# Performance work log

Hardware: AMD Instinct MI355X
Metric: run time of the kernel (lower is better)

The kernel has to match this reference:

```python
import jax, jax.numpy as jnp
import numpy as np

N_LAYER = 2
DEPTH = 2
D_IN = 64
H1 = 64
N = 8192  # sequence length; H2 == N is required by F * chord_mask


def make_chord(n):
    # eye(n) plus, for k in {0,1}, mask[i, (i + 2^k - 1) % n] = 1
    # k=0 re-sets the diagonal; k=1 sets the (wrapped) superdiagonal.
    eye = jnp.eye(n, dtype=jnp.float32)
    superdiag = jnp.roll(eye, 1, axis=1)  # [i, (i+1)%n] = 1
    return jnp.minimum(eye + superdiag, 1.0)


def setup_inputs() -> dict:
    key = jax.random.key(0)
    ks = jax.random.split(key, 8)
    s_in = 1.0 / np.sqrt(D_IN)
    X = jax.random.normal(ks[0], (N, D_IN), dtype=jnp.float32)
    # g stack: DEPTH x Linear(D_IN -> H1) (requires H1 == D_IN to stack)
    g_w = jax.random.uniform(ks[1], (DEPTH, H1, D_IN), jnp.float32, -s_in, s_in)
    g_b = jax.random.uniform(ks[2], (DEPTH, H1), jnp.float32, -s_in, s_in)
    # f stacks, one per layer m: (DEPTH-1) x Linear(D_IN->D_IN), then Linear(D_IN->H2=N)
    f0_w = jax.random.uniform(ks[3], (N_LAYER, D_IN, D_IN), jnp.float32, -s_in, s_in)
    f0_b = jax.random.uniform(ks[4], (N_LAYER, D_IN), jnp.float32, -s_in, s_in)
    fL_w = jax.random.uniform(ks[5], (N_LAYER, N, D_IN), jnp.float32, -s_in, s_in)
    fL_b = jax.random.uniform(ks[6], (N_LAYER, N), jnp.float32, -s_in, s_in)
    return {"X": X, "g_w": g_w, "g_b": g_b, "f0_w": f0_w, "f0_b": f0_b,
            "fL_w": fL_w, "fL_b": fL_b}


def reference(X, g_w, g_b, f0_w, f0_b, fL_w, fL_b):
    chord_mask = make_chord(N)  # [N, N], ~2 nonzeros per row
    # V0 = g stack applied to X
    V = X
    for d in range(DEPTH):
        V = jax.nn.relu(V @ g_w[d].T + g_b[d])  # [N, H1]
    # chained masked-score matmuls
    for m in range(N_LAYER):
        F = jax.nn.relu(X @ f0_w[m].T + f0_b[m])   # [N, D_IN]
        F = jax.nn.relu(F @ fL_w[m].T + fL_b[m])   # [N, N] dense score
        W = F * chord_mask                          # chord-sparse
        V = W @ V                                   # [N, H1]
    return V
```

## Files before the change

kernel.cpp:

```cpp
#include <hip/hip_runtime.h>


#define NROWS 8192
#define BROWS 16
#define RPW 5

__device__ __forceinline__ float rl(float v, int lane) {
  return __int_as_float(__builtin_amdgcn_readlane(__float_as_int(v), lane));
}

__device__ __forceinline__ float wave_sum(float x) {
  x += __int_as_float(__builtin_amdgcn_update_dpp(0, __float_as_int(x), 0x121, 0xF, 0xF, false));
  x += __int_as_float(__builtin_amdgcn_update_dpp(0, __float_as_int(x), 0x122, 0xF, 0xF, false));
  x += __int_as_float(__builtin_amdgcn_update_dpp(0, __float_as_int(x), 0x124, 0xF, 0xF, false));
  x += __int_as_float(__builtin_amdgcn_update_dpp(0, __float_as_int(x), 0x128, 0xF, 0xF, false));
  float a0 = rl(x, 0), a1 = rl(x, 16), a2 = rl(x, 32), a3 = rl(x, 48);
  return (a0 + a1) + (a2 + a3);
}

__device__ __forceinline__ void stageW2(float4 (*Wq)[16][65],
                                        const float* __restrict__ W, int tid) {
  const float4* ws = (const float4*)W;
#pragma unroll
  for (int p = 0; p < 8; ++p) {
    int idx = p * 256 + tid;
    int rem = idx & 1023;
    Wq[idx >> 10][rem & 15][rem >> 4] = ws[idx];
  }
}

template <int R>
__device__ __forceinline__ void mm64_s(const float4 (*Wq)[65], int lane,
                                       const float* __restrict__ X,
                                       const int* growu, float bias, float* acc) {
#pragma unroll
  for (int r = 0; r < R; ++r) acc[r] = bias;
#pragma unroll 4
  for (int kb = 0; kb < 16; ++kb) {
    float4 w4 = Wq[kb][lane];
#pragma unroll
    for (int r = 0; r < R; ++r) {
      float4 xq = *(const float4*)(X + (growu[r] << 6) + (kb << 2));
      acc[r] = fmaf(xq.x, w4.x, acc[r]);
      acc[r] = fmaf(xq.y, w4.y, acc[r]);
      acc[r] = fmaf(xq.z, w4.z, acc[r]);
      acc[r] = fmaf(xq.w, w4.w, acc[r]);
    }
  }
#pragma unroll
  for (int r = 0; r < R; ++r) acc[r] = fmaxf(acc[r], 0.0f);
}

template <int R>
__device__ __forceinline__ void mm64_rl(const float4 (*Wq)[65], int lane,
                                        const float* src, float bias, float* acc) {
#pragma unroll
  for (int r = 0; r < R; ++r) acc[r] = bias;
#pragma unroll 4
  for (int kb = 0; kb < 16; ++kb) {
    float4 w4 = Wq[kb][lane];
#pragma unroll
    for (int r = 0; r < R; ++r) {
      acc[r] = fmaf(rl(src[r], 4 * kb + 0), w4.x, acc[r]);
      acc[r] = fmaf(rl(src[r], 4 * kb + 1), w4.y, acc[r]);
      acc[r] = fmaf(rl(src[r], 4 * kb + 2), w4.z, acc[r]);
      acc[r] = fmaf(rl(src[r], 4 * kb + 3), w4.w, acc[r]);
    }
  }
#pragma unroll
  for (int r = 0; r < R; ++r) acc[r] = fmaxf(acc[r], 0.0f);
}

__global__ __launch_bounds__(256, 2) void fused_smfnet(
    const float* __restrict__ X, const float* __restrict__ g_w,
    const float* __restrict__ g_b, const float* __restrict__ f0_w,
    const float* __restrict__ f0_b, const float* __restrict__ fL_w,
    const float* __restrict__ fL_b, float* __restrict__ out)
{
  __shared__ float4 Wq[2][16][65];
  __shared__ float V0s[20][65];
  __shared__ float V1s[17][65];

  const int tid  = threadIdx.x;
  const int lane = tid & 63;
  const int wv   = tid >> 6;
  const int r0   = blockIdx.x * BROWS;

  stageW2(Wq, g_w, tid);
  float hb  = g_b[lane];
  float vb  = g_b[64 + lane];

  int growu[RPW];
#pragma unroll
  for (int r = 0; r < RPW; ++r) {
    int L = wv * RPW + r;
    growu[r] = __builtin_amdgcn_readfirstlane((r0 + L) & (NROWS - 1));
  }
  __syncthreads();

  float h[RPW];
  mm64_s<RPW>(Wq[0], lane, X, growu, hb, h);

  float v0[RPW];
  mm64_rl<RPW>(Wq[1], lane, h, vb, v0);
#pragma unroll
  for (int r = 0; r < RPW; ++r) V0s[wv * RPW + r][lane] = v0[r];

  __syncthreads();
  stageW2(Wq, f0_w, tid);
  __syncthreads();

  float tb0 = f0_b[lane];
  float t[RPW];
  mm64_s<RPW>(Wq[0], lane, X, growu, tb0, t);

  float v1[RPW];
#pragma unroll
  for (int r = 0; r < RPW; ++r) {
    int L = wv * RPW + r;
    if (L <= 16) {
      int g   = growu[r];
      int gp1 = (g + 1) & (NROWS - 1);
      float pa = wave_sum(t[r] * fL_w[g * 64 + lane]);
      float pb = wave_sum(t[r] * fL_w[gp1 * 64 + lane]);
      float a  = fmaxf(pa + fL_b[g], 0.0f);
      float b  = fmaxf(pb + fL_b[gp1], 0.0f);
      v1[r] = a * v0[r] + b * V0s[L + 1][lane];
      V1s[L][lane] = v1[r];
    }
  }

  __syncthreads();
  float tb1 = f0_b[64 + lane];
  mm64_s<RPW>(Wq[1], lane, X, growu, tb1, t);

  const float* fw1 = fL_w + NROWS * 64;
  const float* fb1 = fL_b + NROWS;
#pragma unroll
  for (int r = 0; r < RPW; ++r) {
    int L = wv * RPW + r;
    if (L <= 15) {
      int g   = growu[r];
      int gp1 = (g + 1) & (NROWS - 1);
      float pa = wave_sum(t[r] * fw1[g * 64 + lane]);
      float pb = wave_sum(t[r] * fw1[gp1 * 64 + lane]);
      float a  = fmaxf(pa + fb1[g], 0.0f);
      float b  = fmaxf(pb + fb1[gp1], 0.0f);
      out[g * 64 + lane] = a * v1[r] + b * V1s[L + 1][lane];
    }
  }
}

extern "C" void kernel_launch(void* const* d_in, const int* in_sizes, int n_in,
                              void* d_out, int out_size, void* d_ws, size_t ws_size,
                              hipStream_t stream) {
  const float* X    = (const float*)d_in[0];
  const float* g_w  = (const float*)d_in[1];
  const float* g_b  = (const float*)d_in[2];
  const float* f0_w = (const float*)d_in[3];
  const float* f0_b = (const float*)d_in[4];
  const float* fL_w = (const float*)d_in[5];
  const float* fL_b = (const float*)d_in[6];
  float* out = (float*)d_out;

  fused_smfnet<<<dim3(NROWS / BROWS), dim3(256), 0, stream>>>(
      X, g_w, g_b, f0_w, f0_b, fL_w, fL_b, out);
}
```

Measured before the change: 85.11 us.

## Prefetch weights into registers, fuse f0 matmuls, and stage h through LDS

Global loads for g_w, f0_w and the fL_w rows each thread needs are issued up front into registers, so their latency overlaps the first matmuls instead of sitting between barriers. The two f0 layer matmuls are fused into one pass that shares the X loads. The second g layer now reads h from shared memory instead of using a readlane per element. The wave reduction uses row_bcast DPP steps rather than four readlanes. Holding the prefetched values in registers raises register pressure under launch_bounds(256,2) and may cause spills.

```diff
diff --git a/kernel.cpp b/kernel.cpp
--- a/kernel.cpp
+++ b/kernel.cpp
@@ -9,24 +9,20 @@
   return __int_as_float(__builtin_amdgcn_readlane(__float_as_int(v), lane));
 }
 
+template <int CTRL, int ROWMASK>
+__device__ __forceinline__ float dppadd(float x) {
+  return __int_as_float(__builtin_amdgcn_update_dpp(
+      0, __float_as_int(x), CTRL, ROWMASK, 0xF, false));
+}
+
 __device__ __forceinline__ float wave_sum(float x) {
-  x += __int_as_float(__builtin_amdgcn_update_dpp(0, __float_as_int(x), 0x121, 0xF, 0xF, false));
-  x += __int_as_float(__builtin_amdgcn_update_dpp(0, __float_as_int(x), 0x122, 0xF, 0xF, false));
-  x += __int_as_float(__builtin_amdgcn_update_dpp(0, __float_as_int(x), 0x124, 0xF, 0xF, false));
-  x += __int_as_float(__builtin_amdgcn_update_dpp(0, __float_as_int(x), 0x128, 0xF, 0xF, false));
-  float a0 = rl(x, 0), a1 = rl(x, 16), a2 = rl(x, 32), a3 = rl(x, 48);
-  return (a0 + a1) + (a2 + a3);
-}
-
-__device__ __forceinline__ void stageW2(float4 (*Wq)[16][65],
-                                        const float* __restrict__ W, int tid) {
-  const float4* ws = (const float4*)W;
-#pragma unroll
-  for (int p = 0; p < 8; ++p) {
-    int idx = p * 256 + tid;
-    int rem = idx & 1023;
-    Wq[idx >> 10][rem & 15][rem >> 4] = ws[idx];
-  }
+  x += dppadd<0x121, 0xF>(x);
+  x += dppadd<0x122, 0xF>(x);
+  x += dppadd<0x124, 0xF>(x);
+  x += dppadd<0x128, 0xF>(x);
+  x += dppadd<0x142, 0xA>(x);
+  x += dppadd<0x143, 0xC>(x);
+  return rl(x, 63);
 }
 
 template <int R>
@@ -52,8 +48,39 @@
 }
 
 template <int R>
-__device__ __forceinline__ void mm64_rl(const float4 (*Wq)[65], int lane,
-                                        const float* src, float bias, float* acc) {
+__device__ __forceinline__ void mm64_x2(const float4 (*W0)[65], const float4 (*W1)[65],
+                                        int lane, const float* __restrict__ X,
+                                        const int* growu, float b0, float b1,
+                                        float* a0, float* a1) {
+#pragma unroll
+  for (int r = 0; r < R; ++r) { a0[r] = b0; a1[r] = b1; }
+#pragma unroll 4
+  for (int kb = 0; kb < 16; ++kb) {
+    float4 w0 = W0[kb][lane];
+    float4 w1 = W1[kb][lane];
+#pragma unroll
+    for (int r = 0; r < R; ++r) {
+      float4 xq = *(const float4*)(X + (growu[r] << 6) + (kb << 2));
+      a0[r] = fmaf(xq.x, w0.x, a0[r]);
+      a0[r] = fmaf(xq.y, w0.y, a0[r]);
+      a0[r] = fmaf(xq.z, w0.z, a0[r]);
+      a0[r] = fmaf(xq.w, w0.w, a0[r]);
+      a1[r] = fmaf(xq.x, w1.x, a1[r]);
+      a1[r] = fmaf(xq.y, w1.y, a1[r]);
+      a1[r] = fmaf(xq.z, w1.z, a1[r]);
+      a1[r] = fmaf(xq.w, w1.w, a1[r]);
+    }
+  }
+#pragma unroll
+  for (int r = 0; r < R; ++r) {
+    a0[r] = fmaxf(a0[r], 0.0f);
+    a1[r] = fmaxf(a1[r], 0.0f);
+  }
+}
+
+template <int R>
+__device__ __forceinline__ void mm64_h(const float4 (*Wq)[65], int lane,
+                                       const float (*Hrow)[64], float bias, float* acc) {
 #pragma unroll
   for (int r = 0; r < R; ++r) acc[r] = bias;
 #pragma unroll 4
@@ -61,10 +88,11 @@
     float4 w4 = Wq[kb][lane];
 #pragma unroll
     for (int r = 0; r < R; ++r) {
-      acc[r] = fmaf(rl(src[r], 4 * kb + 0), w4.x, acc[r]);
-      acc[r] = fmaf(rl(src[r], 4 * kb + 1), w4.y, acc[r]);
-      acc[r] = fmaf(rl(src[r], 4 * kb + 2), w4.z, acc[r]);
-      acc[r] = fmaf(rl(src[r], 4 * kb + 3), w4.w, acc[r]);
+      float4 hq = *(const float4*)(&Hrow[r][kb << 2]);
+      acc[r] = fmaf(hq.x, w4.x, acc[r]);
+      acc[r] = fmaf(hq.y, w4.y, acc[r]);
+      acc[r] = fmaf(hq.z, w4.z, acc[r]);
+      acc[r] = fmaf(hq.w, w4.w, acc[r]);
     }
   }
 #pragma unroll
@@ -80,70 +108,93 @@
   __shared__ float4 Wq[2][16][65];
   __shared__ float V0s[20][65];
   __shared__ float V1s[17][65];
+  __shared__ __align__(16) float Hs[4][RPW][64];
 
   const int tid  = threadIdx.x;
   const int lane = tid & 63;
   const int wv   = tid >> 6;
   const int r0   = blockIdx.x * BROWS;
 
-  stageW2(Wq, g_w, tid);
-  float hb  = g_b[lane];
-  float vb  = g_b[64 + lane];
+  const float4* gq = (const float4*)g_w;
+  float4 gw[8];
+#pragma unroll
+  for (int p = 0; p < 8; ++p) gw[p] = gq[p * 256 + tid];
 
   int growu[RPW];
 #pragma unroll
+  for (int r = 0; r < RPW; ++r)
+    growu[r] = __builtin_amdgcn_readfirstlane((r0 + wv * RPW + r) & (NROWS - 1));
+
+  const float* fw1 = fL_w + NROWS * 64;
+  float fa0[RPW], fb0[RPW], fa1[RPW], fb1v[RPW];
+#pragma unroll
   for (int r = 0; r < RPW; ++r) {
-    int L = wv * RPW + r;
-    growu[r] = __builtin_amdgcn_readfirstlane((r0 + L) & (NROWS - 1));
-  }
+    int g = growu[r], gp1 = (g + 1) & (NROWS - 1);
+    fa0[r]  = fL_w[g * 64 + lane];
+    fb0[r]  = fL_w[gp1 * 64 + lane];
+    fa1[r]  = fw1[g * 64 + lane];
+    fb1v[r] = fw1[gp1 * 64 + lane];
+  }
+
+  const float4* fq = (const float4*)f0_w;
+  float4 fw[8];
+#pragma unroll
+  for (int p = 0; p < 8; ++p) fw[p] = fq[p * 256 + tid];
+
+#pragma unroll
+  for (int p = 0; p < 8; ++p) {
+    int idx = p * 256 + tid, rem = idx & 1023;
+    Wq[idx >> 10][rem & 15][rem >> 4] = gw[p];
+  }
+  float hb = g_b[lane], vb = g_b[64 + lane];
   __syncthreads();
 
   float h[RPW];
   mm64_s<RPW>(Wq[0], lane, X, growu, hb, h);
+#pragma unroll
+  for (int r = 0; r < RPW; ++r) Hs[wv][r][lane] = h[r];
 
   float v0[RPW];
-  mm64_rl<RPW>(Wq[1], lane, h, vb, v0);
+  mm64_h<RPW>(Wq[1], lane, Hs[wv], vb, v0);
 #pragma unroll
   for (int r = 0; r < RPW; ++r) V0s[wv * RPW + r][lane] = v0[r];
-
-  __syncthreads();
-  stageW2(Wq, f0_w, tid);
-  __syncthreads();
-
-  float tb0 = f0_b[lane];
-  float t[RPW];
-  mm64_s<RPW>(Wq[0], lane, X, growu, tb0, t);
+  __syncthreads();
+
+#pragma unroll
+  for (int p = 0; p < 8; ++p) {
+    int idx = p * 256 + tid, rem = idx & 1023;
+    Wq[idx >> 10][rem & 15][rem >> 4] = fw[p];
+  }
+  __syncthreads();
+
+  float t0[RPW], t1[RPW];
+  mm64_x2<RPW>(Wq[0], Wq[1], lane, X, growu,
+               f0_b[lane], f0_b[64 + lane], t0, t1);
 
   float v1[RPW];
 #pragma unroll
   for (int r = 0; r < RPW; ++r) {
     int L = wv * RPW + r;
     if (L <= 16) {
-      int g   = growu[r];
-      int gp1 = (g + 1) & (NROWS - 1);
-      float pa = wave_sum(t[r] * fL_w[g * 64 + lane]);
-      float pb = wave_sum(t[r] * fL_w[gp1 * 64 + lane]);
+      int g = growu[r], gp1 = (g + 1) & (NROWS - 1);
+      float pa = wave_sum(t0[r] * fa0[r]);
+      float pb = wave_sum(t0[r] * fb0[r]);
       float a  = fmaxf(pa + fL_b[g], 0.0f);
       float b  = fmaxf(pb + fL_b[gp1], 0.0f);
       v1[r] = a * v0[r] + b * V0s[L + 1][lane];
       V1s[L][lane] = v1[r];
     }
   }
-
-  __syncthreads();
-  float tb1 = f0_b[64 + lane];
-  mm64_s<RPW>(Wq[1], lane, X, growu, tb1, t);
-
-  const float* fw1 = fL_w + NROWS * 64;
+  __syncthreads();
+
   const float* fb1 = fL_b + NROWS;
 #pragma unroll
   for (int r = 0; r < RPW; ++r) {
     int L = wv * RPW + r;
     if (L <= 15) {
-      int g   = growu[r];
-      int gp1 = (g + 1) & (NROWS - 1);
-      float pa = wave_sum(t[r] * fw1[g * 64 + lane]);
-      float pb = wave_sum(t[r] * fw1[gp1 * 64 + lane]);
+      int g = growu[r], gp1 = (g + 1) & (NROWS - 1);
+      float pa = wave_sum(t1[r] * fa1[r]);
+      float pb = wave_sum(t1[r] * fb1v[r]);
       float a  = fmaxf(pa + fb1[g], 0.0f);
       float b  = fmaxf(pb + fb1[gp1], 0.0f);
       out[g * 64 + lane] = a * v1[r] + b * V1s[L + 1][lane];
```

Result: no change. 85.42 us (+0.4%).
